# Performance work log

Hardware: AMD Instinct MI355X
Metric: run time of the kernel (lower is better)

Reference implementation:

```python
import jax, jax.numpy as jnp
import numpy as np

B, S_IN, IN_DIM, HID, H, W = 256, 2, 2304, 512, 7, 7
SCALE = 1.0 / float(np.sqrt(HID))


def setup_inputs() -> dict:
    key = jax.random.key(0)
    ks = jax.random.split(key, 13)
    w = lambda k, shp: (jax.random.normal(k, shp, dtype=jnp.float32) * 0.02)
    return {
        "status": jax.random.normal(ks[0], (B, S_IN), dtype=jnp.float32),
        "rois": jax.random.uniform(ks[1], (B, 5), dtype=jnp.float32),
        "bbox_feat": jax.random.normal(ks[2], (B, IN_DIM, 1, H, W), dtype=jnp.float32),
        "conv_w": w(ks[3], (HID, IN_DIM, 3, 3)),
        "q1_w": w(ks[4], (HID, S_IN + 4)),
        "k1_w": w(ks[5], (HID, HID)),
        "k2_w": w(ks[6], (HID, HID)),
        "v1_w": w(ks[7], (HID, HID)),
        "v2_w": w(ks[8], (HID, HID)),
        "proj1_w": w(ks[9], (HID, HID)),
        "proj1_b": jnp.zeros((HID,), dtype=jnp.float32),
        "proj2_w": w(ks[10], (HID, HID)),
        "proj2_b": jnp.zeros((HID,), dtype=jnp.float32),
    }


def reference(status, rois, bbox_feat, conv_w, q1_w, k1_w, k2_w, v1_w, v2_w,
              proj1_w, proj1_b, proj2_w, proj2_b):
    x = bbox_feat[:, :, 0]  # squeeze(2) -> [B, IN_DIM, H, W]
    feat = jax.lax.conv_general_dilated(
        x, conv_w, window_strides=(1, 1), padding="SAME",
        dimension_numbers=("NCHW", "OIHW", "NCHW"))  # [B, HID, H, W]
    b, c, h, w_ = feat.shape
    hw = h * w_
    feat_seq = feat.reshape(b, c, hw).transpose(0, 2, 1)  # [B, HW, HID]
    st = jnp.concatenate([status, rois[:, 1:]], axis=1)   # [B, status_dim]
    # query is identical at every spatial position (status broadcast over HW),
    # so attention rows are identical -> compute once per batch element.
    q = st @ q1_w.T  # [B, HID] (forward uses q1 for both branches; q2 is dead code)

    def branch(k_w, v_w, p_w, p_b):
        k = feat_seq @ k_w.T                      # [B, HW, HID]
        v = feat_seq @ v_w.T                      # [B, HW, HID]
        logits = jnp.einsum("bd,bnd->bn", q, k) * SCALE
        att = jax.nn.softmax(logits, axis=-1)     # [B, HW]
        virt = jnp.einsum("bn,bnd->bd", att, v)   # [B, HID]
        virt = virt @ p_w.T + p_b                 # proj (dropout = identity in eval)
        out = feat_seq + virt[:, None, :]         # residual, broadcast over HW
        return out.transpose(0, 2, 1).reshape(b, c, h, w_)[:, :, None]  # [B,HID,1,H,W]

    out1 = branch(k1_w, v1_w, proj1_w, proj1_b)
    out2 = branch(k2_w, v2_w, proj2_w, proj2_b)
    return (out1, out2)
```

## Files before the change

### kernel.cpp

```cpp
#include <hip/hip_runtime.h>
#include <hip/hip_bf16.h>
#include <stdint.h>

#define CIN   2304
#define HID_  512
#define NP    12544
#define OUT1  6422528

typedef float  f32x4 __attribute__((ext_vector_type(4)));
typedef short  s16x8 __attribute__((ext_vector_type(8)));

__device__ __forceinline__ uint16_t f2bf(float f) {
  uint32_t x = __builtin_bit_cast(uint32_t, f);
  return (uint16_t)((x + 0x7FFFu + ((x >> 16) & 1u)) >> 16);
}
__device__ __forceinline__ float bf2f(uint16_t u) {
  return __builtin_bit_cast(float, ((uint32_t)u) << 16);
}
__device__ __forceinline__ void gload16(const void* g, void* l) {
  __builtin_amdgcn_global_load_lds((const __attribute__((address_space(1))) void*)g,
                                   (__attribute__((address_space(3))) void*)l, 16, 0, 0);
}

__global__ __launch_bounds__(256) void prep1_k(const float* __restrict__ xs,
    const float* __restrict__ cw,
    uint16_t* __restrict__ xT, uint16_t* __restrict__ Wt) {
  __shared__ __align__(16) char sm[12800];
  const int tid = threadIdx.x;
  const int bi = blockIdx.x;
  if (bi < 9216) {
    float* t = (float*)sm;
    const int cg = bi % 36, b = bi / 36;
    const int c0 = cg * 64;
    const float4* src = (const float4*)(xs + ((size_t)b * CIN + c0) * 49);
    for (int i = tid; i < 784; i += 256) ((float4*)t)[i] = src[i];
    __syncthreads();
    for (int j = tid; j < 392; j += 256) {
      const int s = j >> 3, cq = j & 7;
      union { uint16_t us[8]; uint4 v; } pk;
#pragma unroll
      for (int q = 0; q < 8; ++q) pk.us[q] = f2bf(t[(cq * 8 + q) * 49 + s]);
      *(uint4*)(xT + ((size_t)(b * 49 + s) * CIN + c0 + cq * 8)) = pk.v;
    }
  } else {
    float* t = (float*)sm;
    const int rest = bi - 9216;
    const int cg = rest % 18, o = rest / 18;
    const int c0 = cg * 128;
    const float* src = cw + ((size_t)o * CIN + c0) * 9;
    for (int i = tid; i < 1152; i += 256) t[i] = src[i];
    __syncthreads();
    if (tid < 144) {
      const int tp = tid >> 4, c8 = tid & 15;
      union { uint16_t us[8]; uint4 v; } pk;
#pragma unroll
      for (int q = 0; q < 8; ++q) pk.us[q] = f2bf(t[(c8 * 8 + q) * 9 + tp]);
      *(uint4*)(Wt + ((size_t)(tp * HID_ + o) * CIN + c0 + c8 * 8)) = pk.v;
    }
  }
}

__device__ __forceinline__ void prep_tail(int rest, int tid, char* sm,
    const float* __restrict__ q1w,
    const float* __restrict__ k1w, const float* __restrict__ k2w,
    const float* __restrict__ v1w, const float* __restrict__ v2w,
    const float* __restrict__ p1w, const float* __restrict__ p2w,
    float* __restrict__ A, float* __restrict__ PVt) {
  if (rest < 16) {
    float* q1s = (float*)sm;
    float (*red)[6][64] = (float(*)[6][64])(sm + 12288);
    const int e0 = (rest & 7) * 64, ib = rest >> 3;
    const int g = tid >> 6, l = tid & 63;
    for (int i = tid; i < 3072; i += 256) q1s[i] = q1w[i];
    __syncthreads();
    const float* kw = (ib ? k2w : k1w) + e0 + l;
    float acc[6] = {};
#pragma unroll 4
    for (int d = g * 128; d < (g + 1) * 128; ++d) {
      const float kv = kw[(size_t)d * 512];
#pragma unroll
      for (int j = 0; j < 6; ++j) acc[j] += q1s[d * 6 + j] * kv;
    }
#pragma unroll
    for (int j = 0; j < 6; ++j) red[g][j][l] = acc[j];
    __syncthreads();
    for (int i2 = tid; i2 < 384; i2 += 256) {
      const int j = i2 >> 6, l2 = i2 & 63;
      A[(ib * 6 + j) * 512 + e0 + l2] =
          red[0][j][l2] + red[1][j][l2] + red[2][j][l2] + red[3][j][l2];
    }
  } else {
    float* Av  = (float*)sm;
    float* Bpt = (float*)(sm + 8192);
    const int r0 = rest - 16;
    const int ibz = r0 >> 6, r2 = r0 & 63;
    const int d0 = (r2 & 7) * 64, e0 = (r2 >> 3) * 64;
    const float* vw = ibz ? v2w : v1w;
    const float* pw = ibz ? p2w : p1w;
    const int tx = tid & 15, ty = tid >> 4;
    float acc[4][4] = {};
    for (int m0 = 0; m0 < 512; m0 += 32) {
      __syncthreads();
      for (int i = tid; i < 2048; i += 256) {
        Av[i] = vw[(size_t)(m0 + (i >> 6)) * 512 + e0 + (i & 63)];
        Bpt[(i & 31) * 68 + (i >> 5)] = pw[(size_t)(d0 + (i >> 5)) * 512 + m0 + (i & 31)];
      }
      __syncthreads();
#pragma unroll 4
      for (int mm = 0; mm < 32; ++mm) {
        const float4 bv = *(const float4*)&Bpt[mm * 68 + tx * 4];
        const float4 av = *(const float4*)&Av[mm * 64 + ty * 4];
        const float a0[4] = {av.x, av.y, av.z, av.w};
        const float b0[4] = {bv.x, bv.y, bv.z, bv.w};
#pragma unroll
        for (int ee = 0; ee < 4; ++ee)
#pragma unroll
          for (int dd = 0; dd < 4; ++dd) acc[ee][dd] += a0[ee] * b0[dd];
      }
    }
#pragma unroll
    for (int ee = 0; ee < 4; ++ee) {
      float4 r; r.x = acc[ee][0]; r.y = acc[ee][1]; r.z = acc[ee][2]; r.w = acc[ee][3];
      *(float4*)&PVt[ibz * 262144 + (size_t)(e0 + ty * 4 + ee) * 512 + d0 + tx * 4] = r;
    }
  }
}

#define LDSX1  11520
#define LDSW   23040
#define LDSZ   47616
__global__ __launch_bounds__(256) void conv_k(const uint16_t* __restrict__ xT,
    const uint16_t* __restrict__ Wt, uint16_t* __restrict__ feat0,
    uint16_t* __restrict__ feat1,
    const float* __restrict__ q1w,
    const float* __restrict__ k1w, const float* __restrict__ k2w,
    const float* __restrict__ v1w, const float* __restrict__ v2w,
    const float* __restrict__ p1w, const float* __restrict__ p2w,
    float* __restrict__ A, float* __restrict__ PVt) {
  __shared__ __align__(16) char lds[47632];
  const int tid = threadIdx.x;
  const int bidx = blockIdx.x;
  if (bidx >= 784) {
    prep_tail(bidx - 784, tid, lds, q1w, k1w, k2w, v1w, v2w, p1w, p2w, A, PVt);
    return;
  }
  const int wid = tid >> 6;
  const int lane = tid & 63;
  const int g16 = (lane >> 4) << 4;
  const int l15 = lane & 15;
  const int ww = wid & 1, wm = wid >> 1;

  const int idx = bidx;
  const int sp = idx & 1;
  const int bn = (idx >> 1) & 3;
  const int bm = idx >> 3;
  const int n0 = bm * 128;
  const int o0 = bn * 128;
  const int c0 = sp * 36;

  const int rb0 = (wm * 64 + l15) * 80 + 640 + g16;
  int maskb[4];
#pragma unroll
  for (int m = 0; m < 4; ++m) {
    const int p = (n0 + wm * 64 + m * 16 + l15) % 49;
    const int y = p / 7, xx = p - y * 7;
    int mb = 0;
#pragma unroll
    for (int t = 0; t < 9; ++t) {
      const int yy = y + t / 3 - 1, xc = xx + t % 3 - 1;
      if (yy >= 0 && yy < 7 && xc >= 0 && xc < 7) mb |= 1 << t;
    }
    maskb[m] = mb;
  }

  const int wb0 = ww * 4096 + l15 * 64 + (g16 ^ (((l15 >> 1) & 3) << 4));

  const char* WtB = (const char*)Wt;
  const char* xTB = (const char*)xT;
  int wsrc[2];
  const int wdstb = wid * 1024;
#pragma unroll
  for (int j = 0; j < 2; ++j) {
    const int slot = j * 256 + tid;
    const int row = slot >> 2, unit = slot & 3;
    const int lu = unit ^ ((row >> 1) & 3);
    wsrc[j] = (o0 + row) * (CIN * 2) + lu * 16;
  }
  int xsrc[3], xv[3];
#pragma unroll
  for (int k = 0; k < 3; ++k) {
    const int slot = k * 256 + tid;
    xv[k] = slot < 720;
    const int row = slot / 5;
    int unit = slot - row * 5; if (unit > 3) unit = 3;
    int nr = n0 - 8 + row;
    nr = nr < 0 ? 0 : (nr > NP - 1 ? NP - 1 : nr);
    xsrc[k] = nr * (CIN * 2) + unit * 16;
  }

  if (tid < 4) *(int*)(lds + LDSZ + tid * 4) = 0;
  __syncthreads();

  {
    const char* xb = xTB + (size_t)c0 * 64;
    if (xv[0]) gload16(xb + xsrc[0], lds + wdstb);
    if (xv[1]) gload16(xb + xsrc[1], lds + 4096 + wdstb);
    if (xv[2]) gload16(xb + xsrc[2], lds + 8192 + wdstb);
    const char* wp0 = WtB + (size_t)c0 * 64;
    gload16(wp0 + wsrc[0], lds + LDSW + wdstb);
    gload16(wp0 + wsrc[1], lds + LDSW + 4096 + wdstb);
    const char* wp1 = WtB + 2359296 + (size_t)c0 * 64;
    gload16(wp1 + wsrc[0], lds + LDSW + 8192 + wdstb);
    gload16(wp1 + wsrc[1], lds + LDSW + 8192 + 4096 + wdstb);
  }

  f32x4 acc[4][4] = {};

#define WISS(TTN, CCO) { \
    const char* wb_ = WtB + (size_t)(TTN) * 2359296 + (size_t)(cc + (CCO)) * 64; \
    const int wo_ = LDSW + ((TTN) % 3) * 8192 + wdstb; \
    gload16(wb_ + wsrc[0], lds + wo_); \
    gload16(wb_ + wsrc[1], lds + wo_ + 4096); }

#define XISS { \
    const char* xb_ = xTB + (size_t)(cc + 1) * 64; \
    const int xo_ = ((cc + 1) & 1) * 11520 + wdstb; \
    if (xv[0]) gload16(xb_ + xsrc[0], lds + xo_); \
    if (xv[1]) gload16(xb_ + xsrc[1], lds + xo_ + 4096); \
    if (xv[2]) gload16(xb_ + xsrc[2], lds + xo_ + 8192); }

#define TAP(TT, VM, ISSUES) \
    asm volatile("s_waitcnt vmcnt(" VM ")" ::: "memory"); \
    __builtin_amdgcn_s_barrier(); \
    __builtin_amdgcn_sched_barrier(0); \
    ISSUES \
    { \
      const int wof_ = LDSW + ((TT) % 3) * 8192; \
      s16x8 bfr_[4]; \
      _Pragma("unroll") \
      for (int n_ = 0; n_ < 4; ++n_) \
        bfr_[n_] = *(const s16x8*)(lds + wof_ + wb0 + n_ * 1024); \
      __builtin_amdgcn_s_setprio(1); \
      _Pragma("unroll") \
      for (int m_ = 0; m_ < 4; ++m_) { \
        const int off_ = m_ * 1280 + (((TT) / 3 - 1) * 7 + ((TT) % 3 - 1)) * 80; \
        const int ab_ = ((maskb[m_] >> (TT)) & 1) ? (rb0 + xsel) : (LDSZ - off_); \
        const s16x8 af_ = *(const s16x8*)(lds + ab_ + off_); \
        _Pragma("unroll") \
        for (int n_ = 0; n_ < 4; ++n_) \
          acc[m_][n_] = __builtin_amdgcn_mfma_f32_16x16x32_bf16(af_, bfr_[n_], acc[m_][n_], 0, 0, 0); \
      } \
      __builtin_amdgcn_s_setprio(0); \
    }

#pragma unroll 1
  for (int cc = c0; cc < c0 + 35; ++cc) {
    const int xsel = (cc & 1) * 11520;
    TAP(0, "2", WISS(2, 0) XISS)
    TAP(1, "5", WISS(3, 0))
    TAP(2, "5", WISS(4, 0))
    TAP(3, "2", WISS(5, 0))
    TAP(4, "2", WISS(6, 0))
    TAP(5, "2", WISS(7, 0))
    TAP(6, "2", WISS(8, 0))
    TAP(7, "2", WISS(0, 1))
    TAP(8, "2", WISS(1, 1))
  }
  {
    const int cc = c0 + 35;
    const int xsel = (cc & 1) * 11520;
    TAP(0, "2", WISS(2, 0))
    TAP(1, "2", WISS(3, 0))
    TAP(2, "2", WISS(4, 0))
    TAP(3, "2", WISS(5, 0))
    TAP(4, "2", WISS(6, 0))
    TAP(5, "2", WISS(7, 0))
    TAP(6, "2", WISS(8, 0))
    TAP(7, "2", )
    TAP(8, "0", )
  }
#undef TAP
#undef WISS
#undef XISS

  uint16_t* fb = (sp ? feat1 : feat0) +
                 ((size_t)(n0 + wm * 64)) * HID_ + o0 + ww * 64;
  const int g4 = (lane >> 4) * 4;
#pragma unroll
  for (int m = 0; m < 4; ++m)
#pragma unroll
    for (int n = 0; n < 4; ++n)
#pragma unroll
      for (int r = 0; r < 4; ++r)
        fb[(m * 16 + g4 + r) * HID_ + n * 16 + l15] = f2bf(acc[m][n][r]);
}

#define FLP 520
__global__ __launch_bounds__(256) void att_k(const uint16_t* __restrict__ feat0,
    const uint16_t* __restrict__ feat1,
    const float* __restrict__ status, const float* __restrict__ rois,
    const float* __restrict__ A, const float* __restrict__ PVt,
    const float* __restrict__ pb1, const float* __restrict__ pb2,
    float* __restrict__ out) {
  __shared__ uint16_t fl[49 * FLP];
  __shared__ float qk[512];
  __shared__ float attv[64];
  __shared__ float fbar[512];
  __shared__ float v2[512];
  __shared__ float part[256];
  const int tid = threadIdx.x;
  const int b = blockIdx.x >> 1, ib = blockIdx.x & 1;

  const uint4* s0 = (const uint4*)(feat0 + (size_t)b * 25088);
  const uint4* s1 = (const uint4*)(feat1 + (size_t)b * 25088);
  for (int i = tid; i < 3136; i += 256) {
    const int n = i >> 6, e8 = (i & 63) << 3;
    union { uint16_t us[8]; uint4 v; } a, c, r;
    a.v = s0[i]; c.v = s1[i];
#pragma unroll
    for (int q = 0; q < 8; ++q) r.us[q] = f2bf(bf2f(a.us[q]) + bf2f(c.us[q]));
    *(uint4*)&fl[n * FLP + e8] = r.v;
  }
  float st6[6];
  st6[0] = status[b * 2]; st6[1] = status[b * 2 + 1];
#pragma unroll
  for (int j = 0; j < 4; ++j) st6[2 + j] = rois[b * 5 + 1 + j];
  for (int e = tid; e < 512; e += 256) {
    const float* Ai = A + ib * 3072;
    float s = 0.f;
#pragma unroll
    for (int j = 0; j < 6; ++j) s += st6[j] * Ai[j * 512 + e];
    qk[e] = s;
  }
  __syncthreads();

  if (tid < 196) {
    const int n = tid >> 2;
    const int e0 = (tid & 3) * 128;
    float s = 0.f;
#pragma unroll 4
    for (int e8 = 0; e8 < 128; e8 += 8) {
      union { uint16_t us[8]; uint4 v; } pk;
      pk.v = *(const uint4*)&fl[n * FLP + e0 + e8];
#pragma unroll
      for (int q = 0; q < 8; ++q) s += bf2f(pk.us[q]) * qk[e0 + e8 + q];
    }
    part[tid] = s;
  }
  __syncthreads();
  if (tid < 64) {
    float l = -1e30f;
    if (tid < 49)
      l = 0.044194173824159216f *
          (part[tid * 4] + part[tid * 4 + 1] + part[tid * 4 + 2] + part[tid * 4 + 3]);
    float mx = l;
#pragma unroll
    for (int o = 32; o > 0; o >>= 1) mx = fmaxf(mx, __shfl_xor(mx, o, 64));
    const float ex = (tid < 49) ? __expf(l - mx) : 0.f;
    float sm = ex;
#pragma unroll
    for (int o = 32; o > 0; o >>= 1) sm += __shfl_xor(sm, o, 64);
    if (tid < 49) attv[tid] = ex / sm;
  }
  __syncthreads();
  for (int e = tid; e < 512; e += 256) {
    float s = 0.f;
#pragma unroll 7
    for (int n = 0; n < 49; ++n) s += attv[n] * bf2f(fl[n * FLP + e]);
    fbar[e] = s;
  }
  __syncthreads();
  for (int d = tid; d < 512; d += 256) {
    const float* P = PVt + ib * 262144 + d;
    float s = (ib ? pb2 : pb1)[d];
#pragma unroll 8
    for (int e = 0; e < 512; ++e) s += P[(size_t)e * 512] * fbar[e];
    v2[d] = s;
  }
  __syncthreads();
  float* ob = out + (size_t)ib * OUT1 + (size_t)b * 25088;
  for (int w = tid; w < 25088; w += 256) {
    const int c = w / 49, p = w - c * 49;
    ob[w] = bf2f(fl[p * FLP + c]) + v2[c];
  }
}

extern "C" void kernel_launch(void* const* d_in, const int* in_sizes, int n_in,
                              void* d_out, int out_size, void* d_ws, size_t ws_size,
                              hipStream_t stream) {
  const float* status = (const float*)d_in[0];
  const float* rois   = (const float*)d_in[1];
  const float* bbox   = (const float*)d_in[2];
  const float* convw  = (const float*)d_in[3];
  const float* q1w    = (const float*)d_in[4];
  const float* k1w    = (const float*)d_in[5];
  const float* k2w    = (const float*)d_in[6];
  const float* v1w    = (const float*)d_in[7];
  const float* v2w    = (const float*)d_in[8];
  const float* p1w    = (const float*)d_in[9];
  const float* p1b    = (const float*)d_in[10];
  const float* p2w    = (const float*)d_in[11];
  const float* p2b    = (const float*)d_in[12];
  float* out = (float*)d_out;
  char* ws = (char*)d_ws;
  uint16_t* xT    = (uint16_t*)(ws);
  uint16_t* Wt    = (uint16_t*)(ws + 57802752);
  uint16_t* feat0 = (uint16_t*)(ws + 79036416);
  uint16_t* feat1 = (uint16_t*)(ws + 91881472);
  float*    PVt   = (float*)(ws + 104726528);
  float*    A     = (float*)(ws + 106823680);
  if (ws_size < 106848256) return;

  hipLaunchKernelGGL(prep1_k, dim3(18432), dim3(256), 0, stream, bbox, convw, xT, Wt);
  hipLaunchKernelGGL(conv_k,  dim3(928),   dim3(256), 0, stream, xT, Wt, feat0, feat1,
                     q1w, k1w, k2w, v1w, v2w, p1w, p2w, A, PVt);
  hipLaunchKernelGGL(att_k,   dim3(512),   dim3(256), 0, stream, feat0, feat1,
                     status, rois, A, PVt, p1b, p2b, out);
}
```

Baseline: 405.5 us.

## Merge both attention branches per block and enlarge prep transpose tiles

Measured after the change: 503.0 us. 1.24x slower.

```diff
diff --git a/kernel.cpp b/kernel.cpp
--- a/kernel.cpp
+++ b/kernel.cpp
@@ -25,26 +25,26 @@
 __global__ __launch_bounds__(256) void prep1_k(const float* __restrict__ xs,
     const float* __restrict__ cw,
     uint16_t* __restrict__ xT, uint16_t* __restrict__ Wt) {
-  __shared__ __align__(16) char sm[12800];
+  __shared__ __align__(16) char sm[56448];
   const int tid = threadIdx.x;
   const int bi = blockIdx.x;
-  if (bi < 9216) {
+  if (bi < 2048) {
     float* t = (float*)sm;
-    const int cg = bi % 36, b = bi / 36;
-    const int c0 = cg * 64;
+    const int b = bi >> 3, cg = bi & 7;
+    const int c0 = cg * 288;
     const float4* src = (const float4*)(xs + ((size_t)b * CIN + c0) * 49);
-    for (int i = tid; i < 784; i += 256) ((float4*)t)[i] = src[i];
+    for (int i = tid; i < 3528; i += 256) ((float4*)t)[i] = src[i];
     __syncthreads();
-    for (int j = tid; j < 392; j += 256) {
-      const int s = j >> 3, cq = j & 7;
+    for (int j = tid; j < 1764; j += 256) {
+      const int s = j / 36, u = j - s * 36;
       union { uint16_t us[8]; uint4 v; } pk;
 #pragma unroll
-      for (int q = 0; q < 8; ++q) pk.us[q] = f2bf(t[(cq * 8 + q) * 49 + s]);
-      *(uint4*)(xT + ((size_t)(b * 49 + s) * CIN + c0 + cq * 8)) = pk.v;
+      for (int q = 0; q < 8; ++q) pk.us[q] = f2bf(t[(u * 8 + q) * 49 + s]);
+      *(uint4*)(xT + ((size_t)(b * 49 + s) * CIN + c0 + u * 8)) = pk.v;
     }
   } else {
     float* t = (float*)sm;
-    const int rest = bi - 9216;
+    const int rest = bi - 2048;
     const int cg = rest % 18, o = rest / 18;
     const int c0 = cg * 128;
     const float* src = cw + ((size_t)o * CIN + c0) * 9;
@@ -303,13 +303,13 @@
     const float* __restrict__ pb1, const float* __restrict__ pb2,
     float* __restrict__ out) {
   __shared__ uint16_t fl[49 * FLP];
-  __shared__ float qk[512];
-  __shared__ float attv[64];
-  __shared__ float fbar[512];
-  __shared__ float v2[512];
-  __shared__ float part[256];
+  __shared__ float qk[2][512];
+  __shared__ float attv[2][64];
+  __shared__ float fbar[2][512];
+  __shared__ float v2[2][512];
+  __shared__ float part[2][196];
   const int tid = threadIdx.x;
-  const int b = blockIdx.x >> 1, ib = blockIdx.x & 1;
+  const int b = blockIdx.x;
 
   const uint4* s0 = (const uint4*)(feat0 + (size_t)b * 25088);
   const uint4* s1 = (const uint4*)(feat1 + (size_t)b * 25088);
@@ -325,63 +325,71 @@
   st6[0] = status[b * 2]; st6[1] = status[b * 2 + 1];
 #pragma unroll
   for (int j = 0; j < 4; ++j) st6[2 + j] = rois[b * 5 + 1 + j];
-  for (int e = tid; e < 512; e += 256) {
+  for (int i2 = tid; i2 < 1024; i2 += 256) {
+    const int ib = i2 >> 9, e = i2 & 511;
     const float* Ai = A + ib * 3072;
     float s = 0.f;
 #pragma unroll
     for (int j = 0; j < 6; ++j) s += st6[j] * Ai[j * 512 + e];
-    qk[e] = s;
-  }
-  __syncthreads();
-
-  if (tid < 196) {
-    const int n = tid >> 2;
-    const int e0 = (tid & 3) * 128;
+    qk[ib][e] = s;
+  }
+  __syncthreads();
+
+  for (int i2 = tid; i2 < 392; i2 += 256) {
+    const int ib = i2 / 196, r = i2 - ib * 196;
+    const int n = r >> 2;
+    const int e0 = (r & 3) * 128;
     float s = 0.f;
 #pragma unroll 4
     for (int e8 = 0; e8 < 128; e8 += 8) {
       union { uint16_t us[8]; uint4 v; } pk;
       pk.v = *(const uint4*)&fl[n * FLP + e0 + e8];
 #pragma unroll
-      for (int q = 0; q < 8; ++q) s += bf2f(pk.us[q]) * qk[e0 + e8 + q];
-    }
-    part[tid] = s;
-  }
-  __syncthreads();
-  if (tid < 64) {
-    float l = -1e30f;
-    if (tid < 49)
-      l = 0.044194173824159216f *
-          (part[tid * 4] + part[tid * 4 + 1] + part[tid * 4 + 2] + part[tid * 4 + 3]);
-    float mx = l;
+      for (int q = 0; q < 8; ++q) s += bf2f(pk.us[q]) * qk[ib][e0 + e8 + q];
+    }
+    part[ib][r] = s;
+  }
+  __syncthreads();
+  if (tid < 128) {
+    const int ib = tid >> 6, l = tid & 63;
+    float lg = -1e30f;
+    if (l < 49)
+      lg = 0.044194173824159216f *
+           (part[ib][l * 4] + part[ib][l * 4 + 1] + part[ib][l * 4 + 2] + part[ib][l * 4 + 3]);
+    float mx = lg;
 #pragma unroll
     for (int o = 32; o > 0; o >>= 1) mx = fmaxf(mx, __shfl_xor(mx, o, 64));
-    const float ex = (tid < 49) ? __expf(l - mx) : 0.f;
+    const float ex = (l < 49) ? __expf(lg - mx) : 0.f;
     float sm = ex;
 #pragma unroll
     for (int o = 32; o > 0; o >>= 1) sm += __shfl_xor(sm, o, 64);
-    if (tid < 49) attv[tid] = ex / sm;
-  }
-  __syncthreads();
-  for (int e = tid; e < 512; e += 256) {
+    if (l < 49) attv[ib][l] = ex / sm;
+  }
+  __syncthreads();
+  for (int i2 = tid; i2 < 1024; i2 += 256) {
+    const int ib = i2 >> 9, e = i2 & 511;
     float s = 0.f;
 #pragma unroll 7
-    for (int n = 0; n < 49; ++n) s += attv[n] * bf2f(fl[n * FLP + e]);
-    fbar[e] = s;
-  }
-  __syncthreads();
-  for (int d = tid; d < 512; d += 256) {
+    for (int n = 0; n < 49; ++n) s += attv[ib][n] * bf2f(fl[n * FLP + e]);
+    fbar[ib][e] = s;
+  }
+  __syncthreads();
+  for (int i2 = tid; i2 < 1024; i2 += 256) {
+    const int ib = i2 >> 9, d = i2 & 511;
     const float* P = PVt + ib * 262144 + d;
     float s = (ib ? pb2 : pb1)[d];
 #pragma unroll 8
-    for (int e = 0; e < 512; ++e) s += P[(size_t)e * 512] * fbar[e];
-    v2[d] = s;
-  }
-  __syncthreads();
-  float* ob = out + (size_t)ib * OUT1 + (size_t)b * 25088;
-  for (int w = tid; w < 25088; w += 256) {
-    const int c = w / 49, p = w - c * 49;
-    ob[w] = bf2f(fl[p * FLP + c]) + v2[c];
+    for (int e = 0; e < 512; ++e) s += P[(size_t)e * 512] * fbar[ib][e];
+    v2[ib][d] = s;
+  }
+  __syncthreads();
+#pragma unroll
+  for (int ib = 0; ib < 2; ++ib) {
+    float* ob = out + (size_t)ib * OUT1 + (size_t)b * 25088;
+    for (int w = tid; w < 25088; w += 256) {
+      const int c = w / 49, p = w - c * 49;
+      ob[w] = bf2f(fl[p * FLP + c]) + v2[ib][c];
+    }
   }
 }
 
@@ -411,9 +419,9 @@
   float*    A     = (float*)(ws + 106823680);
   if (ws_size < 106848256) return;
 
-  hipLaunchKernelGGL(prep1_k, dim3(18432), dim3(256), 0, stream, bbox, convw, xT, Wt);
+  hipLaunchKernelGGL(prep1_k, dim3(11264), dim3(256), 0, stream, bbox, convw, xT, Wt);
   hipLaunchKernelGGL(conv_k,  dim3(928),   dim3(256), 0, stream, xT, Wt, feat0, feat1,
                      q1w, k1w, k2w, v1w, v2w, p1w, p2w, A, PVt);
-  hipLaunchKernelGGL(att_k,   dim3(512),   dim3(256), 0, stream, feat0, feat1,
+  hipLaunchKernelGGL(att_k,   dim3(256),   dim3(256), 0, stream, feat0, feat1,
                      status, rois, A, PVt, p1b, p2b, out);
 }
```
